# Kernel tuning notes

Hardware: AMD Instinct MI355X
Metric: run time of the kernel (lower is better)

## Reference

```python
import jax, jax.numpy as jnp
import numpy as np

B, S, H, KVH, D = 2, 4096, 32, 8, 64
HID = H * D          # 2048
WIN = 256            # sliding window size (incl. self)
CHK = 128            # chunk size for linear attention
NREP = H // KVH


def setup_inputs() -> dict:
    key = jax.random.key(0)
    ks = jax.random.split(key, 5)
    hidden_states = jax.random.normal(ks[0], (B, S, HID), jnp.float32)
    # RoPE tables (Llama-style)
    inv_freq = 1.0 / (10000.0 ** (jnp.arange(0, D, 2, dtype=jnp.float32) / D))
    freqs = jnp.arange(S, dtype=jnp.float32)[:, None] * inv_freq[None, :]
    emb = jnp.concatenate([freqs, freqs], axis=-1)          # [S, D]
    cos = jnp.broadcast_to(jnp.cos(emb)[None], (B, S, D)).astype(jnp.float32)
    sin = jnp.broadcast_to(jnp.sin(emb)[None], (B, S, D)).astype(jnp.float32)
    scale = 0.02
    Wq = jax.random.normal(ks[1], (HID, HID), jnp.float32) * scale
    Wk = jax.random.normal(ks[2], (KVH * D, HID), jnp.float32) * scale
    Wv = jax.random.normal(ks[3], (KVH * D, HID), jnp.float32) * scale
    Wo = jax.random.normal(ks[4], (HID, HID), jnp.float32) * scale
    return {"hidden_states": hidden_states, "cos": cos, "sin": sin,
            "Wq": Wq, "Wk": Wk, "Wv": Wv, "Wo": Wo}


def rotate_half(x):
    x1, x2 = jnp.split(x, 2, axis=-1)
    return jnp.concatenate([-x2, x1], axis=-1)


def local_window_attention(q, k, v):
    nb = S // WIN
    qb = q.reshape(B, H, nb, WIN, D)
    kb = k.reshape(B, H, nb, WIN, D)
    vb = v.reshape(B, H, nb, WIN, D)
    zpad = jnp.zeros_like(kb[:, :, :1])
    kcat = jnp.concatenate([jnp.concatenate([zpad, kb[:, :, :-1]], axis=2), kb], axis=3)  # [B,H,nb,2W,D]
    vcat = jnp.concatenate([jnp.concatenate([zpad, vb[:, :, :-1]], axis=2), vb], axis=3)
    scores = jnp.einsum('bhnqd,bhnkd->bhnqk', qb, kcat) / jnp.sqrt(jnp.float32(D))
    i = jnp.arange(WIN)[:, None]          # query pos within block
    j = jnp.arange(2 * WIN)[None, :]      # key pos within concat window
    diff = i + WIN - j                    # q_abs - key_abs
    base = (diff >= 0) & (diff < WIN)     # causal + window
    n = jnp.arange(nb)[:, None, None]
    valid = (n * WIN + j[None] - WIN) >= 0   # key_abs >= 0 (mask block-0 padding)
    mask = base[None] & valid                # [nb, W, 2W]
    scores = jnp.where(mask[None, None], scores, -1e30)
    attn = jax.nn.softmax(scores, axis=-1)
    out = jnp.einsum('bhnqk,bhnkd->bhnqd', attn, vcat)
    return out.reshape(B, H, S, D)


def linear_memory_attention(q, k, v):
    # causal linear attention with elu+1 feature map, chunked prefix state
    phi = lambda x: jax.nn.elu(x) + 1.0
    nc = S // CHK
    pq = phi(q).reshape(B, H, nc, CHK, D)
    pk = phi(k).reshape(B, H, nc, CHK, D)
    vc = v.reshape(B, H, nc, CHK, D)
    # intra-chunk (causal within chunk)
    cm = jnp.tril(jnp.ones((CHK, CHK), bool))
    scores = jnp.einsum('bhncd,bhnkd->bhnck', pq, pk)
    scores = jnp.where(cm, scores, 0.0)
    num = jnp.einsum('bhnck,bhnkd->bhncd', scores, vc)
    den = scores.sum(-1)
    # inter-chunk via exclusive prefix sums of KV state
    kv = jnp.einsum('bhnkd,bhnke->bhnde', pk, vc)      # [B,H,nc,D,D]
    ks = pk.sum(axis=3)                                # [B,H,nc,D]
    z4 = jnp.zeros_like(kv[:, :, :1])
    Sprev = jnp.concatenate([z4, jnp.cumsum(kv, axis=2)[:, :, :-1]], axis=2)
    z3 = jnp.zeros_like(ks[:, :, :1])
    zprev = jnp.concatenate([z3, jnp.cumsum(ks, axis=2)[:, :, :-1]], axis=2)
    num = num + jnp.einsum('bhncd,bhnde->bhnce', pq, Sprev)
    den = den + jnp.einsum('bhncd,bhnd->bhnc', pq, zprev)
    out = num / (den[..., None] + 1e-6)
    return out.reshape(B, H, S, D)


def reference(hidden_states, cos, sin, Wq, Wk, Wv, Wo):
    q = jnp.einsum('bsh,oh->bso', hidden_states, Wq).reshape(B, S, H, D).transpose(0, 2, 1, 3)
    k = jnp.einsum('bsh,oh->bso', hidden_states, Wk).reshape(B, S, KVH, D).transpose(0, 2, 1, 3)
    v = jnp.einsum('bsh,oh->bso', hidden_states, Wv).reshape(B, S, KVH, D).transpose(0, 2, 1, 3)
    c = cos[:, None]  # [B,1,S,D]
    s = sin[:, None]
    q = q * c + rotate_half(q) * s
    k = k * c + rotate_half(k) * s
    k = jnp.repeat(k, NREP, axis=1)
    v = jnp.repeat(v, NREP, axis=1)
    local_out = local_window_attention(q, k, v)
    linear_out = linear_memory_attention(q, k, v)
    hybrid = 0.5 * local_out + 0.5 * linear_out              # [B,H,S,D]
    hybrid = hybrid.transpose(0, 2, 1, 3).reshape(B, S, HID)
    return jnp.einsum('bsh,oh->bso', hybrid, Wo)
```

## Files before the change

### kernel.cpp

```cpp
#include <hip/hip_runtime.h>

#define gB 2
#define gS 4096
#define gH 32
#define gKVH 8
#define gHID 2048
#define gNC 32
#define gBS (gB*gS)

using bf16x8 = __attribute__((ext_vector_type(8))) short;
using f32x4  = __attribute__((ext_vector_type(4))) float;

__device__ __forceinline__ float bf2f(unsigned short u){
  return __uint_as_float(((unsigned)u) << 16);
}
__device__ __forceinline__ unsigned short f2bf(float f){
  unsigned u = __float_as_uint(f);
  u = (u + 0x7fffu + ((u >> 16) & 1u)) >> 16;
  return (unsigned short)u;
}
__device__ __forceinline__ float phi_f(float x){ return x > 0.f ? x + 1.f : __expf(x); }

__device__ __forceinline__ void unpack8(uint4 v, unsigned short* o){
  o[0]=(unsigned short)(v.x&0xffffu); o[1]=(unsigned short)(v.x>>16);
  o[2]=(unsigned short)(v.y&0xffffu); o[3]=(unsigned short)(v.y>>16);
  o[4]=(unsigned short)(v.z&0xffffu); o[5]=(unsigned short)(v.z>>16);
  o[6]=(unsigned short)(v.w&0xffffu); o[7]=(unsigned short)(v.w>>16);
}
__device__ __forceinline__ uint4 pack8(const unsigned short* s){
  uint4 v;
  v.x = (unsigned)s[0] | ((unsigned)s[1]<<16);
  v.y = (unsigned)s[2] | ((unsigned)s[3]<<16);
  v.z = (unsigned)s[4] | ((unsigned)s[5]<<16);
  v.w = (unsigned)s[6] | ((unsigned)s[7]<<16);
  return v;
}

typedef const __attribute__((address_space(1))) void* gas_ptr;
typedef __attribute__((address_space(3))) void* las_ptr;
__device__ __forceinline__ void gload16(const void* g, void* l){
  __builtin_amdgcn_global_load_lds((gas_ptr)g, (las_ptr)l, 16, 0, 0);
}

__global__ void cvt_kernel(const float* __restrict__ in, unsigned short* __restrict__ out, int n){
  int stride = gridDim.x * blockDim.x;
  for (int i = blockIdx.x*blockDim.x + threadIdx.x; i*4 < n; i += stride){
    float4 v = *(const float4*)(in + (size_t)i*4);
    ushort4 o;
    o.x = f2bf(v.x); o.y = f2bf(v.y); o.z = f2bf(v.z); o.w = f2bf(v.w);
    *(ushort4*)(out + (size_t)i*4) = o;
  }
}

__global__ __launch_bounds__(512, 2) void gemm_qkv(const unsigned short* __restrict__ A,
                                                   const unsigned short* __restrict__ Bm,
                                                   const float* __restrict__ cosb,
                                                   const float* __restrict__ sinb,
                                                   unsigned short* __restrict__ q_r,
                                                   unsigned short* __restrict__ k_r,
                                                   unsigned short* __restrict__ vproj)
{
  const int Kdim = 2048;
  __shared__ unsigned short Sh[2*24576];
  int tid = threadIdx.x, lane = tid & 63, w = tid >> 6, lr = lane & 15, lg = lane >> 4;
  int wm = w >> 2, wn = w & 3;
  const int ntn = 12;
  int nwg = gridDim.x;
  int bid = (int)blockIdx.x;
  int swz = (bid & 7) * (nwg >> 3) + (bid >> 3);
  long m0 = (long)(swz / ntn) * 128;
  long n0 = (long)(swz % ntn) * 256;
  const int NT = Kdim >> 6;

  f32x4 acc[4][4] = {};

  auto stage = [&](int t){
    int sbase = (t & 1) * 24576;
    int k0 = t << 6;
    #pragma unroll
    for (int i = 0; i < 2; ++i){
      int c = w*64 + lane + i*512;
      int row = c >> 3, g = c & 7;
      int colb = (g ^ (row & 7)) << 4;
      gload16((const char*)A + ((m0 + row) * (long)Kdim + k0) * 2 + colb,
              (void*)&Sh[sbase + (w*64 + i*512)*8]);
    }
    #pragma unroll
    for (int i = 0; i < 4; ++i){
      int c = w*64 + lane + i*512;
      int row = c >> 3, g = c & 7;
      int colb = (g ^ (row & 7)) << 4;
      gload16((const char*)Bm + ((n0 + row) * (long)Kdim + k0) * 2 + colb,
              (void*)&Sh[sbase + 8192 + (w*64 + i*512)*8]);
    }
  };

  stage(0);
  for (int t = 0; t < NT; ++t){
    asm volatile("s_waitcnt vmcnt(0)" ::: "memory");
    __builtin_amdgcn_s_barrier();
    if (t + 1 < NT) stage(t + 1);
    int sb = (t & 1) * 24576;
    #pragma unroll
    for (int kk = 0; kk < 2; ++kk){
      bf16x8 af[4], bfr[4];
      #pragma unroll
      for (int m = 0; m < 4; ++m){
        int row = wm*64 + m*16 + lr;
        af[m] = *(const bf16x8*)&Sh[sb + row*64 + (((kk*4 + lg) ^ (row & 7)) << 3)];
      }
      #pragma unroll
      for (int n = 0; n < 4; ++n){
        int row = wn*64 + n*16 + lr;
        bfr[n] = *(const bf16x8*)&Sh[sb + 8192 + row*64 + (((kk*4 + lg) ^ (row & 7)) << 3)];
      }
      __builtin_amdgcn_s_setprio(1);
      #pragma unroll
      for (int m = 0; m < 4; ++m)
        #pragma unroll
        for (int n = 0; n < 4; ++n)
          acc[m][n] = __builtin_amdgcn_mfma_f32_16x16x32_bf16(af[m], bfr[n], acc[m][n], 0, 0, 0);
      __builtin_amdgcn_s_setprio(0);
    }
  }

  long colbase = n0 + wn*64;
  if (colbase < 2048){
    int head = (int)(colbase >> 6);
    #pragma unroll
    for (int m = 0; m < 4; ++m)
      #pragma unroll
      for (int r = 0; r < 4; ++r){
        long srow = m0 + wm*64 + m*16 + 4*lg + r;
        int b = (int)(srow >> 12), s = (int)(srow & 4095);
        const float* cp = cosb + srow*64;
        const float* sp = sinb + srow*64;
        unsigned short* op = q_r + ((size_t)(b*gH + head)*gS + s)*64;
        #pragma unroll
        for (int n = 0; n < 2; ++n){
          int d = n*16 + lr;
          float x1 = acc[m][n][r], x2 = acc[m][n+2][r];
          op[d]      = f2bf(x1*cp[d]    - x2*sp[d]);
          op[d+32]   = f2bf(x2*cp[d+32] + x1*sp[d+32]);
        }
      }
  } else if (colbase < 2560){
    int head = (int)(colbase >> 6) - 32;
    #pragma unroll
    for (int m = 0; m < 4; ++m)
      #pragma unroll
      for (int r = 0; r < 4; ++r){
        long srow = m0 + wm*64 + m*16 + 4*lg + r;
        int b = (int)(srow >> 12), s = (int)(srow & 4095);
        const float* cp = cosb + srow*64;
        const float* sp = sinb + srow*64;
        unsigned short* op = k_r + ((size_t)(b*gKVH + head)*gS + s)*64;
        #pragma unroll
        for (int n = 0; n < 2; ++n){
          int d = n*16 + lr;
          float x1 = acc[m][n][r], x2 = acc[m][n+2][r];
          op[d]      = f2bf(x1*cp[d]    - x2*sp[d]);
          op[d+32]   = f2bf(x2*cp[d+32] + x1*sp[d+32]);
        }
      }
  } else {
    #pragma unroll
    for (int m = 0; m < 4; ++m)
      #pragma unroll
      for (int r = 0; r < 4; ++r){
        long srow = m0 + wm*64 + m*16 + 4*lg + r;
        unsigned short* op = vproj + (size_t)srow*512 + (colbase - 2560);
        #pragma unroll
        for (int n = 0; n < 4; ++n)
          op[n*16 + lr] = f2bf(acc[m][n][r]);
      }
  }
}

template<int OUT_BF16>
__global__ __launch_bounds__(512, 2) void gemm256(const unsigned short* __restrict__ A,
                                                  const unsigned short* __restrict__ Bm,
                                                  void* __restrict__ Cout,
                                                  int Mdim, int Ndim, int Kdim)
{
  __shared__ unsigned short Sh[2*32768];
  int tid = threadIdx.x, lane = tid & 63, w = tid >> 6, lr = lane & 15, lg = lane >> 4;
  int wm = w >> 2, wn = w & 3;
  int ntn = Ndim >> 8;
  int nwg = gridDim.x;
  int bid = (int)blockIdx.x;
  int swz = (bid & 7) * (nwg >> 3) + (bid >> 3);
  long m0 = (long)(swz / ntn) * 256;
  long n0 = (long)(swz % ntn) * 256;
  int NT = Kdim >> 6;

  f32x4 acc[8][4] = {};

  auto stage = [&](int t){
    int sbase = (t & 1) * 32768;
    int k0 = t << 6;
    #pragma unroll
    for (int i = 0; i < 4; ++i){
      int c = w*64 + lane + i*512;
      int row = c >> 3, g = c & 7;
      int colb = (g ^ (row & 7)) << 4;
      gload16((const char*)A + ((m0 + row) * (long)Kdim + k0) * 2 + colb,
              (void*)&Sh[sbase + (w*64 + i*512)*8]);
      gload16((const char*)Bm + ((n0 + row) * (long)Kdim + k0) * 2 + colb,
              (void*)&Sh[sbase + 16384 + (w*64 + i*512)*8]);
    }
  };

  stage(0);
  for (int t = 0; t < NT; ++t){
    asm volatile("s_waitcnt vmcnt(0)" ::: "memory");
    __builtin_amdgcn_s_barrier();
    if (t + 1 < NT) stage(t + 1);
    int sb = (t & 1) * 32768;
    #pragma unroll
    for (int kk = 0; kk < 2; ++kk){
      bf16x8 af[8], bfr[4];
      #pragma unroll
      for (int m = 0; m < 8; ++m){
        int row = wm*128 + m*16 + lr;
        af[m] = *(const bf16x8*)&Sh[sb + row*64 + (((kk*4 + lg) ^ (row & 7)) << 3)];
      }
      #pragma unroll
      for (int n = 0; n < 4; ++n){
        int row = wn*64 + n*16 + lr;
        bfr[n] = *(const bf16x8*)&Sh[sb + 16384 + row*64 + (((kk*4 + lg) ^ (row & 7)) << 3)];
      }
      __builtin_amdgcn_s_setprio(1);
      #pragma unroll
      for (int m = 0; m < 8; ++m)
        #pragma unroll
        for (int n = 0; n < 4; ++n)
          acc[m][n] = __builtin_amdgcn_mfma_f32_16x16x32_bf16(af[m], bfr[n], acc[m][n], 0, 0, 0);
      __builtin_amdgcn_s_setprio(0);
    }
  }

  #pragma unroll
  for (int m = 0; m < 8; ++m)
    #pragma unroll
    for (int n = 0; n < 4; ++n)
      #pragma unroll
      for (int r = 0; r < 4; ++r){
        long row = m0 + wm*128 + m*16 + 4*lg + r;
        long col = n0 + wn*64 + n*16 + lr;
        float v = acc[m][n][r];
        if (OUT_BF16) ((unsigned short*)Cout)[row*Ndim + col] = f2bf(v);
        else          ((float*)Cout)[row*Ndim + col] = v;
      }
}

__global__ __launch_bounds__(256) void transpose64(const unsigned short* __restrict__ in,
                                                   unsigned short* __restrict__ out,
                                                   int tokStride, int voff, int mode)
{
  __shared__ unsigned short T[64*72];
  int bid = blockIdx.x;
  int st = bid & 63; int kvh = (bid >> 6) & 7; int b = bid >> 9;
  int s0 = st*64;
  int tid = threadIdx.x;
  const unsigned short* ip;
  size_t tokstr;
  if (mode == 0){ ip = in + ((size_t)(b*gKVH+kvh)*gS + s0)*64;                  tokstr = 64; }
  else          { ip = in + (size_t)(b*gS+s0)*tokStride + voff + kvh*64;        tokstr = tokStride; }
  #pragma unroll
  for (int i = 0; i < 2; ++i){
    int cc = tid + 256*i; int sl = cc >> 3, ch = cc & 7;
    *(uint4*)&T[sl*72 + ch*8] = *(const uint4*)&ip[(size_t)sl*tokstr + ch*8];
  }
  __syncthreads();
  unsigned short* op = out + ((size_t)(b*gKVH+kvh)*64)*gS;
  #pragma unroll
  for (int i = 0; i < 2; ++i){
    int cc = tid + 256*i; int d = cc >> 3, ch = cc & 7;
    unsigned short t[8];
    #pragma unroll
    for (int u = 0; u < 8; ++u) t[u] = T[(ch*8+u)*72 + d];
    *(uint4*)&op[(size_t)d*gS + s0 + ch*8] = pack8(t);
  }
}

__global__ __launch_bounds__(512) void local_attn(const unsigned short* __restrict__ q_r,
                                                  const unsigned short* __restrict__ k_r,
                                                  const unsigned short* __restrict__ vt,
                                                  unsigned short* __restrict__ olocal)
{
  __shared__ unsigned short Qs[128*72];
  __shared__ unsigned short Ks[2][64*72];
  __shared__ unsigned short VTs[2][64*72];
  __shared__ unsigned short Ps[8*16*72];
  int bid = blockIdx.x;
  int qt = bid & 31; int h = (bid >> 5) & 31; int b = bid >> 10;
  int kvh = h >> 2;
  int q0 = qt*128;
  int tid = threadIdx.x, lane = tid & 63, w = tid >> 6, lr = lane & 15, lg = lane >> 4;
  const unsigned short* qp = q_r + ((size_t)(b*gH  +h  )*gS + q0)*64;
  const unsigned short* kp = k_r + ((size_t)(b*gKVH+kvh)*gS)*64;
  const unsigned short* vp = vt  + ((size_t)(b*gKVH+kvh)*64)*gS;

  #pragma unroll
  for (int i = 0; i < 2; ++i){
    int cc = tid + 512*i; int row = cc >> 3, ch = cc & 7;
    *(uint4*)&Qs[row*72 + ch*8] = *(const uint4*)&qp[row*64 + ch*8];
  }

  int kt0 = (q0 >= 256) ? 0 : ((256 - q0) >> 6);
  int krow = tid >> 3, kch = tid & 7;
  uint4 kreg, vreg;
  {
    int kb = q0 - 256 + kt0*64;
    kreg = *(const uint4*)&kp[(size_t)(kb+krow)*64 + kch*8];
    vreg = *(const uint4*)&vp[(size_t)krow*gS + kb + kch*8];
    *(uint4*)&Ks[0][krow*72 + kch*8]  = kreg;
    *(uint4*)&VTs[0][krow*72 + kch*8] = vreg;
  }

  float psum[4] = {0.f, 0.f, 0.f, 0.f};
  f32x4 accO[4] = {};
  int wq = w*16;

  for (int kt = kt0; kt < 6; ++kt){
    int cur = (kt - kt0) & 1;
    __syncthreads();
    bool more = (kt + 1 < 6);
    if (more){
      int kb2 = q0 - 256 + (kt+1)*64;
      kreg = *(const uint4*)&kp[(size_t)(kb2+krow)*64 + kch*8];
      vreg = *(const uint4*)&vp[(size_t)krow*gS + kb2 + kch*8];
    }

    f32x4 sc[4] = {};
    #pragma unroll
    for (int kk = 0; kk < 64; kk += 32){
      bf16x8 aq = *(const bf16x8*)&Qs[(wq+lr)*72 + kk + 8*lg];
      #pragma unroll
      for (int f = 0; f < 4; ++f){
        bf16x8 bk = *(const bf16x8*)&Ks[cur][(f*16+lr)*72 + kk + 8*lg];
        sc[f] = __builtin_amdgcn_mfma_f32_16x16x32_bf16(aq, bk, sc[f], 0, 0, 0);
      }
    }
    #pragma unroll
    for (int f = 0; f < 4; ++f)
      #pragma unroll
      for (int r = 0; r < 4; ++r){
        int i = wq + 4*lg + r;
        int j = kt*64 + f*16 + lr;
        bool keep = (j > i) && (j <= i + 256);
        float e = __expf(sc[f][r] * 0.125f);
        float p = keep ? e : 0.f;
        psum[r] += p;
        Ps[w*1152 + (4*lg + r)*72 + f*16 + lr] = f2bf(p);
      }
    #pragma unroll
    for (int kk = 0; kk < 64; kk += 32){
      bf16x8 ap = *(const bf16x8*)&Ps[w*1152 + lr*72 + kk + 8*lg];
      #pragma unroll
      for (int dt = 0; dt < 4; ++dt){
        bf16x8 bv = *(const bf16x8*)&VTs[cur][(dt*16+lr)*72 + kk + 8*lg];
        accO[dt] = __builtin_amdgcn_mfma_f32_16x16x32_bf16(ap, bv, accO[dt], 0, 0, 0);
      }
    }
    if (more){
      *(uint4*)&Ks[cur^1][krow*72 + kch*8]  = kreg;
      *(uint4*)&VTs[cur^1][krow*72 + kch*8] = vreg;
    }
  }
  #pragma unroll
  for (int off = 1; off < 16; off <<= 1)
    #pragma unroll
    for (int r = 0; r < 4; ++r) psum[r] += __shfl_xor(psum[r], off);
  #pragma unroll
  for (int dt = 0; dt < 4; ++dt)
    #pragma unroll
    for (int r = 0; r < 4; ++r){
      int s = q0 + wq + 4*lg + r;
      int d = dt*16 + lr;
      float o = accO[dt][r] / psum[r];
      olocal[((size_t)(b*gS+s)*gH + h)*64 + d] = f2bf(0.5f * o);
    }
}

__global__ __launch_bounds__(256) void lin_pass1(const unsigned short* __restrict__ ktr,
                                                 const unsigned short* __restrict__ vt,
                                                 float* __restrict__ kvbuf, float* __restrict__ ksbuf)
{
  __shared__ unsigned short pkT[64*136];
  __shared__ unsigned short vT[64*136];
  int bid = blockIdx.x;
  int c = bid & 31; int kvh = (bid >> 5) & 7; int b = bid >> 8;
  int tid = threadIdx.x, lane = tid & 63, w = tid >> 6, lr = lane & 15, lg = lane >> 4;
  int s0 = c*128;
  const unsigned short* kp = ktr + ((size_t)(b*gKVH+kvh)*64)*gS;
  const unsigned short* vp = vt  + ((size_t)(b*gKVH+kvh)*64)*gS;
  #pragma unroll
  for (int i = 0; i < 4; ++i){
    int cc = tid + 256*i; int d = cc >> 4, ch = cc & 15;
    unsigned short t[8]; unpack8(*(const uint4*)&kp[(size_t)d*gS + s0 + ch*8], t);
    #pragma unroll
    for (int u = 0; u < 8; ++u) t[u] = f2bf(phi_f(bf2f(t[u])));
    *(uint4*)&pkT[d*136 + ch*8] = pack8(t);
    *(uint4*)&vT[d*136 + ch*8]  = *(const uint4*)&vp[(size_t)d*gS + s0 + ch*8];
  }
  __syncthreads();
  f32x4 acc[4] = {};
  #pragma unroll
  for (int kk = 0; kk < 128; kk += 32){
    bf16x8 a = *(const bf16x8*)&pkT[(16*w+lr)*136 + kk + 8*lg];
    #pragma unroll
    for (int et = 0; et < 4; ++et){
      bf16x8 bv = *(const bf16x8*)&vT[(16*et+lr)*136 + kk + 8*lg];
      acc[et] = __builtin_amdgcn_mfma_f32_16x16x32_bf16(a, bv, acc[et], 0, 0, 0);
    }
  }
  size_t base = (size_t)((b*gKVH+kvh)*gNC + c);
  float* kvp = kvbuf + base*4096;
  #pragma unroll
  for (int et = 0; et < 4; ++et)
    #pragma unroll
    for (int r = 0; r < 4; ++r)
      kvp[(16*w + 4*lg + r)*64 + 16*et + lr] = acc[et][r];
  if (tid < 64){
    float sum = 0.f;
    for (int k = 0; k < 128; ++k) sum += bf2f(pkT[tid*136 + k]);
    ksbuf[base*64 + tid] = sum;
  }
}

__global__ void lin_pass2(const float* __restrict__ kvin, float* __restrict__ kvout,
                          float* __restrict__ ksbuf){
  int t = blockIdx.x*256 + threadIdx.x;
  const int per = 4096 + 64;
  if (t >= gB*gKVH*per) return;
  int bh = t / per; int e = t % per;
  if (e < 4096){
    int d = e >> 6, ecol = e & 63;
    const float* p = kvin  + (size_t)bh*gNC*4096 + e;
    float* q       = kvout + (size_t)bh*gNC*4096 + ecol*64 + d;
    float acc = 0.f;
    for (int cix = 0; cix < gNC; ++cix){ float v = p[(size_t)cix*4096]; q[(size_t)cix*4096] = acc; acc += v; }
  } else {
    float* p = ksbuf + (size_t)bh*gNC*64 + (e - 4096);
    float acc = 0.f;
    for (int cix = 0; cix < gNC; ++cix){ float v = p[cix*64]; p[cix*64] = acc; acc += v; }
  }
}

__global__ __launch_bounds__(256) void lin_pass3(const unsigned short* __restrict__ q_r,
                                                 const unsigned short* __restrict__ k_r,
                                                 const unsigned short* __restrict__ vt,
                                                 const float* __restrict__ SprevT,
                                                 const float* __restrict__ zprev,
                                                 const unsigned short* __restrict__ olocal,
                                                 unsigned short* __restrict__ hout)
{
  __shared__ unsigned short pq[128*72];
  __shared__ unsigned short pk[64*72];
  __shared__ unsigned short Ph[128*72];
  __shared__ unsigned short vT[64*72];
  __shared__ unsigned short SpT[64*72];
  __shared__ float zp[64];

  int bid = blockIdx.x;
  int c = bid & 31; int h = (bid >> 5) & 31; int b = bid >> 10;
  int kvh = h >> 2;
  int tid = threadIdx.x, lane = tid & 63, w = tid >> 6, lr = lane & 15, lg = lane >> 4;
  int s0 = c*128;
  const unsigned short* qp = q_r + ((size_t)(b*gH  +h  )*gS + s0)*64;
  const unsigned short* kp = k_r + ((size_t)(b*gKVH+kvh)*gS + s0)*64;
  const unsigned short* vp = vt  + ((size_t)(b*gKVH+kvh)*64)*gS;
  const float* Sp  = SprevT + ((size_t)((b*gKVH+kvh)*gNC + c))*4096;
  const float* zpg = zprev  + ((size_t)((b*gKVH+kvh)*gNC + c))*64;

  #pragma unroll
  for (int i = 0; i < 4; ++i){
    int cc = tid + 256*i; int row = cc >> 3, d0 = (cc & 7)*8;
    unsigned short t[8]; unpack8(*(const uint4*)(qp + row*64 + d0), t);
    #pragma unroll
    for (int u = 0; u < 8; ++u) pq[row*72 + d0 + u] = f2bf(phi_f(bf2f(t[u])));
  }
  #pragma unroll
  for (int i = 0; i < 16; ++i){
    int f = tid + 256*i; int e = f >> 6, d = f & 63;
    SpT[e*72 + d] = f2bf(Sp[f]);
  }
  if (tid < 64) zp[tid] = zpg[tid];

  float den[2][4] = {};
  f32x4 accO[2][4] = {};

  for (int kh = 0; kh < 2; ++kh){
    __syncthreads();
    #pragma unroll
    for (int i = 0; i < 2; ++i){
      int cc = tid + 256*i; int kr = cc >> 3, d0 = (cc & 7)*8;
      unsigned short t[8]; unpack8(*(const uint4*)(kp + (kh*64+kr)*64 + d0), t);
      #pragma unroll
      for (int u = 0; u < 8; ++u) pk[kr*72 + d0 + u] = f2bf(phi_f(bf2f(t[u])));
      *(uint4*)&vT[kr*72 + d0] = *(const uint4*)&vp[(size_t)kr*gS + s0 + kh*64 + d0];
    }
    __syncthreads();

    f32x4 sc[2][4] = {};
    #pragma unroll
    for (int kk = 0; kk < 64; kk += 32){
      bf16x8 a[2];
      #pragma unroll
      for (int rt = 0; rt < 2; ++rt) a[rt] = *(const bf16x8*)&pq[(32*w+16*rt+lr)*72 + kk + 8*lg];
      #pragma unroll
      for (int ct = 0; ct < 4; ++ct){
        bf16x8 bk = *(const bf16x8*)&pk[(16*ct+lr)*72 + kk + 8*lg];
        #pragma unroll
        for (int rt = 0; rt < 2; ++rt)
          sc[rt][ct] = __builtin_amdgcn_mfma_f32_16x16x32_bf16(a[rt], bk, sc[rt][ct], 0, 0, 0);
      }
    }
    #pragma unroll
    for (int rt = 0; rt < 2; ++rt)
      #pragma unroll
      for (int ct = 0; ct < 4; ++ct)
        #pragma unroll
        for (int r = 0; r < 4; ++r){
          int qrow = 32*w + 16*rt + 4*lg + r;
          int krow = kh*64 + 16*ct + lr;
          float sv = (krow <= qrow) ? sc[rt][ct][r] : 0.f;
          den[rt][r] += sv;
          Ph[qrow*72 + 16*ct + lr] = f2bf(sv);
        }
    #pragma unroll
    for (int kk = 0; kk < 64; kk += 32){
      bf16x8 ap[2];
      #pragma unroll
      for (int rt = 0; rt < 2; ++rt) ap[rt] = *(const bf16x8*)&Ph[(32*w+16*rt+lr)*72 + kk + 8*lg];
      #pragma unroll
      for (int et = 0; et < 4; ++et){
        bf16x8 bv = *(const bf16x8*)&vT[(16*et+lr)*72 + kk + 8*lg];
        #pragma unroll
        for (int rt = 0; rt < 2; ++rt)
          accO[rt][et] = __builtin_amdgcn_mfma_f32_16x16x32_bf16(ap[rt], bv, accO[rt][et], 0, 0, 0);
      }
    }
  }
  #pragma unroll
  for (int kk = 0; kk < 64; kk += 32){
    bf16x8 a[2];
    #pragma unroll
    for (int rt = 0; rt < 2; ++rt) a[rt] = *(const bf16x8*)&pq[(32*w+16*rt+lr)*72 + kk + 8*lg];
    #pragma unroll
    for (int et = 0; et < 4; ++et){
      bf16x8 bs = *(const bf16x8*)&SpT[(16*et+lr)*72 + kk + 8*lg];
      #pragma unroll
      for (int rt = 0; rt < 2; ++rt)
        accO[rt][et] = __builtin_amdgcn_mfma_f32_16x16x32_bf16(a[rt], bs, accO[rt][et], 0, 0, 0);
    }
  }
  #pragma unroll
  for (int rt = 0; rt < 2; ++rt)
    #pragma unroll
    for (int r = 0; r < 4; ++r){
      int qrow = 32*w + 16*rt + 4*lg + r;
      float part = 0.f;
      #pragma unroll
      for (int u = 0; u < 4; ++u){
        int d = 4*lr + u;
        part += bf2f(pq[qrow*72 + d]) * zp[d];
      }
      den[rt][r] += part;
      #pragma unroll
      for (int off = 1; off < 16; off <<= 1)
        den[rt][r] += __shfl_xor(den[rt][r], off);
    }
  #pragma unroll
  for (int rt = 0; rt < 2; ++rt)
    #pragma unroll
    for (int et = 0; et < 4; ++et)
      #pragma unroll
      for (int r = 0; r < 4; ++r){
        int qrow = 32*w + 16*rt + 4*lg + r;
        int e = 16*et + lr;
        float o = accO[rt][et][r] / (den[rt][r] + 1e-6f);
        int s = s0 + qrow;
        size_t idx = ((size_t)(b*gS+s)*gH + h)*64 + e;
        hout[idx] = f2bf(bf2f(olocal[idx]) + 0.5f * o);
      }
}

extern "C" void kernel_launch(void* const* d_in, const int* in_sizes, int n_in,
                              void* d_out, int out_size, void* d_ws, size_t ws_size,
                              hipStream_t stream)
{
  const float* hidden = (const float*)d_in[0];
  const float* cosb   = (const float*)d_in[1];
  const float* sinb   = (const float*)d_in[2];
  const float* Wq     = (const float*)d_in[3];
  const float* Wk     = (const float*)d_in[4];
  const float* Wv     = (const float*)d_in[5];
  const float* Wo     = (const float*)d_in[6];
  float* out = (float*)d_out;

  char* ws = (char*)d_ws;
  size_t off = 0;
  auto alloc = [&](size_t bytes)->void*{
    void* p = ws + off; off += (bytes + 255) & ~(size_t)255; return p;
  };
  unsigned short* hbf    = (unsigned short*)alloc((size_t)gBS*gHID*2);
  unsigned short* wqkv   = (unsigned short*)alloc((size_t)3072*gHID*2);
  unsigned short* wob    = (unsigned short*)alloc((size_t)gHID*gHID*2);
  unsigned short* vproj  = (unsigned short*)alloc((size_t)gBS*512*2);
  unsigned short* q_r    = (unsigned short*)alloc((size_t)gBS*gHID*2);
  unsigned short* k_r    = (unsigned short*)alloc((size_t)gBS*512*2);
  unsigned short* ktr    = (unsigned short*)alloc((size_t)gBS*512*2);
  unsigned short* vt     = (unsigned short*)alloc((size_t)gBS*512*2);
  unsigned short* olocal = (unsigned short*)alloc((size_t)gBS*gHID*2);
  float* kvbuf           = (float*)alloc((size_t)gB*gKVH*gNC*4096*4);
  float* kvT             = (float*)alloc((size_t)gB*gKVH*gNC*4096*4);
  float* ksbuf           = (float*)alloc((size_t)gB*gKVH*gNC*64*4);

  auto cvt = [&](const float* in, unsigned short* o, int n){
    int nb = (n/4 + 255)/256; if (nb > 4096) nb = 4096;
    cvt_kernel<<<dim3(nb), dim3(256), 0, stream>>>(in, o, n);
  };
  cvt(hidden, hbf, gBS*gHID);
  cvt(Wq, wqkv, gHID*gHID);
  cvt(Wk, wqkv + (size_t)2048*gHID, 512*gHID);
  cvt(Wv, wqkv + (size_t)2560*gHID, 512*gHID);
  cvt(Wo, wob, gHID*gHID);

  gemm_qkv<<<dim3(64*12), dim3(512), 0, stream>>>(hbf, wqkv, cosb, sinb, q_r, k_r, vproj);

  transpose64<<<dim3(gB*gKVH*64), dim3(256), 0, stream>>>(k_r,   ktr, 64,  0, 0);
  transpose64<<<dim3(gB*gKVH*64), dim3(256), 0, stream>>>(vproj, vt,  512, 0, 1);

  local_attn<<<dim3(gB*gH*32), dim3(512), 0, stream>>>(q_r, k_r, vt, olocal);
  lin_pass1<<<dim3(gB*gKVH*gNC), dim3(256), 0, stream>>>(ktr, vt, kvbuf, ksbuf);
  lin_pass2<<<dim3((gB*gKVH*(4096+64) + 255)/256), dim3(256), 0, stream>>>(kvbuf, kvT, ksbuf);
  lin_pass3<<<dim3(gB*gH*gNC), dim3(256), 0, stream>>>(q_r, k_r, vt, kvT, ksbuf, olocal, hbf);

  gemm256<0><<<dim3(32*8), dim3(512), 0, stream>>>(hbf, wob, (void*)out, 8192, 2048, 2048);
}
```

Before: 352.0 us.

## Unify QKV and output GEMMs into a finer-grained pipelined 256x256 kernel

Replaces the separate QKV GEMM (128x256 tiles) and output GEMM with one templated 256x256-tile kernel. Each K step is split into four quarter-tile load units interleaved with four MFMA phases, prefetching up to two steps ahead and waiting with partial vmcnt counts instead of draining all loads every step. The QKV GEMM now uses larger tiles, which halves its grid and raises data reuse, at the cost of fewer workgroups and more barriers per step. The finer interleaving is meant to hide global-load latency behind compute.

```diff
diff --git a/kernel.cpp b/kernel.cpp
--- a/kernel.cpp
+++ b/kernel.cpp
@@ -52,137 +52,18 @@
   }
 }
 
-__global__ __launch_bounds__(512, 2) void gemm_qkv(const unsigned short* __restrict__ A,
-                                                   const unsigned short* __restrict__ Bm,
-                                                   const float* __restrict__ cosb,
-                                                   const float* __restrict__ sinb,
-                                                   unsigned short* __restrict__ q_r,
-                                                   unsigned short* __restrict__ k_r,
-                                                   unsigned short* __restrict__ vproj)
+template<int ROPE>
+__global__ __launch_bounds__(512, 2) void gemm8p(const unsigned short* __restrict__ A,
+                                                 const unsigned short* __restrict__ Bm,
+                                                 const float* __restrict__ cosb,
+                                                 const float* __restrict__ sinb,
+                                                 unsigned short* __restrict__ q_r,
+                                                 unsigned short* __restrict__ k_r,
+                                                 unsigned short* __restrict__ vproj,
+                                                 float* __restrict__ Cout,
+                                                 int Ndim)
 {
   const int Kdim = 2048;
-  __shared__ unsigned short Sh[2*24576];
-  int tid = threadIdx.x, lane = tid & 63, w = tid >> 6, lr = lane & 15, lg = lane >> 4;
-  int wm = w >> 2, wn = w & 3;
-  const int ntn = 12;
-  int nwg = gridDim.x;
-  int bid = (int)blockIdx.x;
-  int swz = (bid & 7) * (nwg >> 3) + (bid >> 3);
-  long m0 = (long)(swz / ntn) * 128;
-  long n0 = (long)(swz % ntn) * 256;
-  const int NT = Kdim >> 6;
-
-  f32x4 acc[4][4] = {};
-
-  auto stage = [&](int t){
-    int sbase = (t & 1) * 24576;
-    int k0 = t << 6;
-    #pragma unroll
-    for (int i = 0; i < 2; ++i){
-      int c = w*64 + lane + i*512;
-      int row = c >> 3, g = c & 7;
-      int colb = (g ^ (row & 7)) << 4;
-      gload16((const char*)A + ((m0 + row) * (long)Kdim + k0) * 2 + colb,
-              (void*)&Sh[sbase + (w*64 + i*512)*8]);
-    }
-    #pragma unroll
-    for (int i = 0; i < 4; ++i){
-      int c = w*64 + lane + i*512;
-      int row = c >> 3, g = c & 7;
-      int colb = (g ^ (row & 7)) << 4;
-      gload16((const char*)Bm + ((n0 + row) * (long)Kdim + k0) * 2 + colb,
-              (void*)&Sh[sbase + 8192 + (w*64 + i*512)*8]);
-    }
-  };
-
-  stage(0);
-  for (int t = 0; t < NT; ++t){
-    asm volatile("s_waitcnt vmcnt(0)" ::: "memory");
-    __builtin_amdgcn_s_barrier();
-    if (t + 1 < NT) stage(t + 1);
-    int sb = (t & 1) * 24576;
-    #pragma unroll
-    for (int kk = 0; kk < 2; ++kk){
-      bf16x8 af[4], bfr[4];
-      #pragma unroll
-      for (int m = 0; m < 4; ++m){
-        int row = wm*64 + m*16 + lr;
-        af[m] = *(const bf16x8*)&Sh[sb + row*64 + (((kk*4 + lg) ^ (row & 7)) << 3)];
-      }
-      #pragma unroll
-      for (int n = 0; n < 4; ++n){
-        int row = wn*64 + n*16 + lr;
-        bfr[n] = *(const bf16x8*)&Sh[sb + 8192 + row*64 + (((kk*4 + lg) ^ (row & 7)) << 3)];
-      }
-      __builtin_amdgcn_s_setprio(1);
-      #pragma unroll
-      for (int m = 0; m < 4; ++m)
-        #pragma unroll
-        for (int n = 0; n < 4; ++n)
-          acc[m][n] = __builtin_amdgcn_mfma_f32_16x16x32_bf16(af[m], bfr[n], acc[m][n], 0, 0, 0);
-      __builtin_amdgcn_s_setprio(0);
-    }
-  }
-
-  long colbase = n0 + wn*64;
-  if (colbase < 2048){
-    int head = (int)(colbase >> 6);
-    #pragma unroll
-    for (int m = 0; m < 4; ++m)
-      #pragma unroll
-      for (int r = 0; r < 4; ++r){
-        long srow = m0 + wm*64 + m*16 + 4*lg + r;
-        int b = (int)(srow >> 12), s = (int)(srow & 4095);
-        const float* cp = cosb + srow*64;
-        const float* sp = sinb + srow*64;
-        unsigned short* op = q_r + ((size_t)(b*gH + head)*gS + s)*64;
-        #pragma unroll
-        for (int n = 0; n < 2; ++n){
-          int d = n*16 + lr;
-          float x1 = acc[m][n][r], x2 = acc[m][n+2][r];
-          op[d]      = f2bf(x1*cp[d]    - x2*sp[d]);
-          op[d+32]   = f2bf(x2*cp[d+32] + x1*sp[d+32]);
-        }
-      }
-  } else if (colbase < 2560){
-    int head = (int)(colbase >> 6) - 32;
-    #pragma unroll
-    for (int m = 0; m < 4; ++m)
-      #pragma unroll
-      for (int r = 0; r < 4; ++r){
-        long srow = m0 + wm*64 + m*16 + 4*lg + r;
-        int b = (int)(srow >> 12), s = (int)(srow & 4095);
-        const float* cp = cosb + srow*64;
-        const float* sp = sinb + srow*64;
-        unsigned short* op = k_r + ((size_t)(b*gKVH + head)*gS + s)*64;
-        #pragma unroll
-        for (int n = 0; n < 2; ++n){
-          int d = n*16 + lr;
-          float x1 = acc[m][n][r], x2 = acc[m][n+2][r];
-          op[d]      = f2bf(x1*cp[d]    - x2*sp[d]);
-          op[d+32]   = f2bf(x2*cp[d+32] + x1*sp[d+32]);
-        }
-      }
-  } else {
-    #pragma unroll
-    for (int m = 0; m < 4; ++m)
-      #pragma unroll
-      for (int r = 0; r < 4; ++r){
-        long srow = m0 + wm*64 + m*16 + 4*lg + r;
-        unsigned short* op = vproj + (size_t)srow*512 + (colbase - 2560);
-        #pragma unroll
-        for (int n = 0; n < 4; ++n)
-          op[n*16 + lr] = f2bf(acc[m][n][r]);
-      }
-  }
-}
-
-template<int OUT_BF16>
-__global__ __launch_bounds__(512, 2) void gemm256(const unsigned short* __restrict__ A,
-                                                  const unsigned short* __restrict__ Bm,
-                                                  void* __restrict__ Cout,
-                                                  int Mdim, int Ndim, int Kdim)
-{
   __shared__ unsigned short Sh[2*32768];
   int tid = threadIdx.x, lane = tid & 63, w = tid >> 6, lr = lane & 15, lg = lane >> 4;
   int wm = w >> 2, wn = w & 3;
@@ -192,66 +73,169 @@
   int swz = (bid & 7) * (nwg >> 3) + (bid >> 3);
   long m0 = (long)(swz / ntn) * 256;
   long n0 = (long)(swz % ntn) * 256;
-  int NT = Kdim >> 6;
+  const int NT = Kdim >> 6;
 
   f32x4 acc[8][4] = {};
 
-  auto stage = [&](int t){
-    int sbase = (t & 1) * 32768;
+  auto stageU = [&](int t, int unit){
+    int sb = (t & 1) * 32768;
     int k0 = t << 6;
-    #pragma unroll
-    for (int i = 0; i < 4; ++i){
+    const unsigned short* G = (unit < 2) ? A : Bm;
+    long r0 = (unit < 2) ? m0 : n0;
+    int rowbase = (unit & 1) * 128;
+    int regionOff = sb + ((unit < 2) ? 0 : 16384) + rowbase*64;
+    #pragma unroll
+    for (int i = 0; i < 2; ++i){
       int c = w*64 + lane + i*512;
-      int row = c >> 3, g = c & 7;
+      int row = rowbase + (c >> 3), g = c & 7;
       int colb = (g ^ (row & 7)) << 4;
-      gload16((const char*)A + ((m0 + row) * (long)Kdim + k0) * 2 + colb,
-              (void*)&Sh[sbase + (w*64 + i*512)*8]);
-      gload16((const char*)Bm + ((n0 + row) * (long)Kdim + k0) * 2 + colb,
-              (void*)&Sh[sbase + 16384 + (w*64 + i*512)*8]);
+      gload16((const char*)G + ((r0 + row) * (long)Kdim + k0) * 2 + colb,
+              (void*)&Sh[regionOff + c*8]);
     }
   };
 
-  stage(0);
+  stageU(0,0); stageU(0,1); stageU(0,2); stageU(0,3);
+  stageU(1,0); stageU(1,1);
+  asm volatile("s_waitcnt vmcnt(4)" ::: "memory");
+  __builtin_amdgcn_s_barrier();
+
   for (int t = 0; t < NT; ++t){
-    asm volatile("s_waitcnt vmcnt(0)" ::: "memory");
+    int sb = (t & 1) * 32768;
+    bf16x8 a[8][2], bl[2][2];
+
+    #pragma unroll
+    for (int mg = 0; mg < 8; ++mg){
+      int row = wm*128 + mg*16 + lr;
+      a[mg][0] = *(const bf16x8*)&Sh[sb + row*64 + ((lg ^ (row & 7)) << 3)];
+    }
+    #pragma unroll
+    for (int nf = 0; nf < 2; ++nf){
+      int row = wn*64 + nf*16 + lr;
+      #pragma unroll
+      for (int kk = 0; kk < 2; ++kk)
+        bl[nf][kk] = *(const bf16x8*)&Sh[sb + 16384 + row*64 + (((kk*4 + lg) ^ (row & 7)) << 3)];
+    }
+    if (t + 1 < NT) stageU(t+1, 2);
+    __builtin_amdgcn_s_setprio(1);
+    #pragma unroll
+    for (int mg = 0; mg < 8; ++mg)
+      #pragma unroll
+      for (int nf = 0; nf < 2; ++nf)
+        acc[mg][nf] = __builtin_amdgcn_mfma_f32_16x16x32_bf16(a[mg][0], bl[nf][0], acc[mg][nf], 0, 0, 0);
+    __builtin_amdgcn_s_setprio(0);
     __builtin_amdgcn_s_barrier();
-    if (t + 1 < NT) stage(t + 1);
-    int sb = (t & 1) * 32768;
-    #pragma unroll
-    for (int kk = 0; kk < 2; ++kk){
-      bf16x8 af[8], bfr[4];
-      #pragma unroll
-      for (int m = 0; m < 8; ++m){
-        int row = wm*128 + m*16 + lr;
-        af[m] = *(const bf16x8*)&Sh[sb + row*64 + (((kk*4 + lg) ^ (row & 7)) << 3)];
-      }
-      #pragma unroll
-      for (int n = 0; n < 4; ++n){
-        int row = wn*64 + n*16 + lr;
-        bfr[n] = *(const bf16x8*)&Sh[sb + 16384 + row*64 + (((kk*4 + lg) ^ (row & 7)) << 3)];
-      }
-      __builtin_amdgcn_s_setprio(1);
+
+    #pragma unroll
+    for (int mg = 0; mg < 8; ++mg){
+      int row = wm*128 + mg*16 + lr;
+      a[mg][1] = *(const bf16x8*)&Sh[sb + row*64 + (((4 + lg) ^ (row & 7)) << 3)];
+    }
+    if (t + 1 < NT) stageU(t+1, 3);
+    __builtin_amdgcn_s_setprio(1);
+    #pragma unroll
+    for (int mg = 0; mg < 8; ++mg)
+      #pragma unroll
+      for (int nf = 0; nf < 2; ++nf)
+        acc[mg][nf] = __builtin_amdgcn_mfma_f32_16x16x32_bf16(a[mg][1], bl[nf][1], acc[mg][nf], 0, 0, 0);
+    __builtin_amdgcn_s_setprio(0);
+    __builtin_amdgcn_s_barrier();
+
+    #pragma unroll
+    for (int nf = 0; nf < 2; ++nf){
+      int row = wn*64 + (nf+2)*16 + lr;
+      #pragma unroll
+      for (int kk = 0; kk < 2; ++kk)
+        bl[nf][kk] = *(const bf16x8*)&Sh[sb + 16384 + row*64 + (((kk*4 + lg) ^ (row & 7)) << 3)];
+    }
+    if (t + 2 < NT) stageU(t+2, 0);
+    __builtin_amdgcn_s_setprio(1);
+    #pragma unroll
+    for (int mg = 0; mg < 8; ++mg)
+      #pragma unroll
+      for (int nf = 0; nf < 2; ++nf)
+        acc[mg][nf+2] = __builtin_amdgcn_mfma_f32_16x16x32_bf16(a[mg][0], bl[nf][0], acc[mg][nf+2], 0, 0, 0);
+    __builtin_amdgcn_s_setprio(0);
+    __builtin_amdgcn_s_barrier();
+
+    if (t + 2 < NT) stageU(t+2, 1);
+    __builtin_amdgcn_s_setprio(1);
+    #pragma unroll
+    for (int mg = 0; mg < 8; ++mg)
+      #pragma unroll
+      for (int nf = 0; nf < 2; ++nf)
+        acc[mg][nf+2] = __builtin_amdgcn_mfma_f32_16x16x32_bf16(a[mg][1], bl[nf][1], acc[mg][nf+2], 0, 0, 0);
+    __builtin_amdgcn_s_setprio(0);
+    if (t + 1 < NT){
+      if (t + 1 == NT - 1) asm volatile("s_waitcnt vmcnt(0)" ::: "memory");
+      else                 asm volatile("s_waitcnt vmcnt(4)" ::: "memory");
+    }
+    __builtin_amdgcn_s_barrier();
+  }
+
+  if (ROPE){
+    long colbase = n0 + wn*64;
+    if (colbase < 2048){
+      int head = (int)(colbase >> 6);
       #pragma unroll
       for (int m = 0; m < 8; ++m)
         #pragma unroll
-        for (int n = 0; n < 4; ++n)
-          acc[m][n] = __builtin_amdgcn_mfma_f32_16x16x32_bf16(af[m], bfr[n], acc[m][n], 0, 0, 0);
-      __builtin_amdgcn_s_setprio(0);
-    }
-  }
-
-  #pragma unroll
-  for (int m = 0; m < 8; ++m)
-    #pragma unroll
-    for (int n = 0; n < 4; ++n)
-      #pragma unroll
-      for (int r = 0; r < 4; ++r){
-        long row = m0 + wm*128 + m*16 + 4*lg + r;
-        long col = n0 + wn*64 + n*16 + lr;
-        float v = acc[m][n][r];
-        if (OUT_BF16) ((unsigned short*)Cout)[row*Ndim + col] = f2bf(v);
-        else          ((float*)Cout)[row*Ndim + col] = v;
-      }
+        for (int r = 0; r < 4; ++r){
+          long srow = m0 + wm*128 + m*16 + 4*lg + r;
+          int b = (int)(srow >> 12), s = (int)(srow & 4095);
+          const float* cp = cosb + srow*64;
+          const float* sp = sinb + srow*64;
+          unsigned short* op = q_r + ((size_t)(b*gH + head)*gS + s)*64;
+          #pragma unroll
+          for (int n = 0; n < 2; ++n){
+            int d = n*16 + lr;
+            float x1 = acc[m][n][r], x2 = acc[m][n+2][r];
+            op[d]      = f2bf(x1*cp[d]    - x2*sp[d]);
+            op[d+32]   = f2bf(x2*cp[d+32] + x1*sp[d+32]);
+          }
+        }
+    } else if (colbase < 2560){
+      int head = (int)(colbase >> 6) - 32;
+      #pragma unroll
+      for (int m = 0; m < 8; ++m)
+        #pragma unroll
+        for (int r = 0; r < 4; ++r){
+          long srow = m0 + wm*128 + m*16 + 4*lg + r;
+          int b = (int)(srow >> 12), s = (int)(srow & 4095);
+          const float* cp = cosb + srow*64;
+          const float* sp = sinb + srow*64;
+          unsigned short* op = k_r + ((size_t)(b*gKVH + head)*gS + s)*64;
+          #pragma unroll
+          for (int n = 0; n < 2; ++n){
+            int d = n*16 + lr;
+            float x1 = acc[m][n][r], x2 = acc[m][n+2][r];
+            op[d]      = f2bf(x1*cp[d]    - x2*sp[d]);
+            op[d+32]   = f2bf(x2*cp[d+32] + x1*sp[d+32]);
+          }
+        }
+    } else {
+      #pragma unroll
+      for (int m = 0; m < 8; ++m)
+        #pragma unroll
+        for (int r = 0; r < 4; ++r){
+          long srow = m0 + wm*128 + m*16 + 4*lg + r;
+          unsigned short* op = vproj + (size_t)srow*512 + (colbase - 2560);
+          #pragma unroll
+          for (int n = 0; n < 4; ++n)
+            op[n*16 + lr] = f2bf(acc[m][n][r]);
+        }
+    }
+  } else {
+    #pragma unroll
+    for (int m = 0; m < 8; ++m)
+      #pragma unroll
+      for (int n = 0; n < 4; ++n)
+        #pragma unroll
+        for (int r = 0; r < 4; ++r){
+          long row = m0 + wm*128 + m*16 + 4*lg + r;
+          long col = n0 + wn*64 + n*16 + lr;
+          Cout[row*Ndim + col] = acc[m][n][r];
+        }
+  }
 }
 
 __global__ __launch_bounds__(256) void transpose64(const unsigned short* __restrict__ in,
@@ -629,7 +613,8 @@
   cvt(Wv, wqkv + (size_t)2560*gHID, 512*gHID);
   cvt(Wo, wob, gHID*gHID);
 
-  gemm_qkv<<<dim3(64*12), dim3(512), 0, stream>>>(hbf, wqkv, cosb, sinb, q_r, k_r, vproj);
+  gemm8p<1><<<dim3(32*12), dim3(512), 0, stream>>>(hbf, wqkv, cosb, sinb,
+                                                   q_r, k_r, vproj, nullptr, 3072);
 
   transpose64<<<dim3(gB*gKVH*64), dim3(256), 0, stream>>>(k_r,   ktr, 64,  0, 0);
   transpose64<<<dim3(gB*gKVH*64), dim3(256), 0, stream>>>(vproj, vt,  512, 0, 1);
@@ -639,5 +624,6 @@
   lin_pass2<<<dim3((gB*gKVH*(4096+64) + 255)/256), dim3(256), 0, stream>>>(kvbuf, kvT, ksbuf);
   lin_pass3<<<dim3(gB*gH*gNC), dim3(256), 0, stream>>>(q_r, k_r, vt, kvT, ksbuf, olocal, hbf);
 
-  gemm256<0><<<dim3(32*8), dim3(512), 0, stream>>>(hbf, wob, (void*)out, 8192, 2048, 2048);
-}
+  gemm8p<0><<<dim3(32*8), dim3(512), 0, stream>>>(hbf, wob, nullptr, nullptr,
+                                                  nullptr, nullptr, nullptr, out, 2048);
+}
```

Result: slower. 376.7 us (+7.0%).
